# Kernel optimization log

Hardware: AMD Instinct MI355X
Metric: run time of the kernel (lower is better)

Reference implementation:

```python
import jax, jax.numpy as jnp
import numpy as np

NUM_HEADS = 8
CHANNELS = 512


def setup_inputs() -> dict:
    key = jax.random.key(0)
    k1, k2, k3, k4, k5 = jax.random.split(key, 5)
    C = CHANNELS
    x = jax.random.normal(k1, (8, C, 64, 64), dtype=jnp.float32)
    # 1x1 conv weights stored as (out_ch, in_ch) matrices
    qkv_w = jax.random.normal(k2, (3 * C, C), dtype=jnp.float32) * (C ** -0.5)
    qkv_b = jax.random.normal(k3, (3 * C,), dtype=jnp.float32) * 0.02
    proj_w = jax.random.normal(k4, (C, C), dtype=jnp.float32) * (C ** -0.5)
    proj_b = jax.random.normal(k5, (C,), dtype=jnp.float32) * 0.02
    return {"x": x, "qkv_w": qkv_w, "qkv_b": qkv_b, "proj_w": proj_w, "proj_b": proj_b}


def reference(x, qkv_w, qkv_b, proj_w, proj_b):
    B, C, H, W = x.shape
    heads = NUM_HEADS
    d = C // heads
    N = H * W
    scale = d ** -0.5
    # 1x1 conv == per-pixel matmul over channels
    qkv = jnp.einsum('bchw,oc->bohw', x, qkv_w) + qkv_b[None, :, None, None]
    qkv = qkv.reshape(B, 3, heads, d, N)
    q, k, v = qkv[:, 0], qkv[:, 1], qkv[:, 2]  # each (B, heads, d, N)
    # NOTE: attention over the channel dim -> (B, heads, d, d), as in the torch code
    attn = jax.nn.softmax(jnp.einsum('bhdn,bhen->bhde', q, k) * scale, axis=-1)
    # dropout is identity in eval mode
    out = jnp.einsum('bhde,bhen->bhdn', attn, v).reshape(B, C, H, W)
    out = jnp.einsum('bchw,oc->bohw', out, proj_w) + proj_b[None, :, None, None]
    return out, attn.mean(axis=1)  # (B,C,H,W), (B,d,d)
```

## Files before the change

### kernel.cpp

```cpp
#include <hip/hip_runtime.h>
#include <cstdio>
#include <cstdint>

#define BATCH 8
#define CH    512
#define OC3   1536
#define QKROWS 1024
#define NPIX  4096
#define HEADS 8
#define HDIM  64
#define KDEPTH 512
#define SCALE 0.125f
#define NSPLIT 16

typedef __bf16 bf16;
typedef __bf16 bf16x4 __attribute__((ext_vector_type(4)));
typedef __bf16 bf16x8 __attribute__((ext_vector_type(8)));
typedef float  f32x4  __attribute__((ext_vector_type(4)));

__global__ __launch_bounds__(256) void convert_bf16_kernel(
    const float* __restrict__ in, bf16* __restrict__ out, int n)
{
    const int i = blockIdx.x * 256 + threadIdx.x;
    if (i < n) out[i] = (bf16)in[i];
}

__global__ __launch_bounds__(256) void transpose_convert_kernel(
    const float* __restrict__ src, bf16* __restrict__ dst, size_t src_bstride)
{
    const int b  = blockIdx.z;
    const int n0 = blockIdx.x * 64;
    const int c0 = blockIdx.y * 64;
    __shared__ float tile[64][65];
    const int t = threadIdx.x;
    const float* xp = src + (size_t)b * src_bstride;

    #pragma unroll
    for (int i = 0; i < 4; ++i) {
        const int lin = t + 256 * i;
        const int r   = lin >> 4;
        const int c4  = (lin & 15) * 4;
        const float4 v = *(const float4*)(xp + (size_t)(c0 + r) * 4096 + n0 + c4);
        tile[r][c4 + 0] = v.x; tile[r][c4 + 1] = v.y;
        tile[r][c4 + 2] = v.z; tile[r][c4 + 3] = v.w;
    }
    __syncthreads();

    bf16* op = dst + (size_t)b * 4096 * 512;
    #pragma unroll
    for (int i = 0; i < 2; ++i) {
        const int lin = t + 256 * i;
        const int n   = lin >> 3;
        const int c8  = (lin & 7) * 8;
        bf16x8 v;
        #pragma unroll
        for (int jj = 0; jj < 8; ++jj) v[jj] = (bf16)tile[c8 + jj][n];
        *(bf16x8*)(op + (size_t)(n0 + n) * 512 + c0 + c8) = v;
    }
}

__global__ __launch_bounds__(256) void mfma_gemm_kernel(
    const bf16* __restrict__ A, const bf16* __restrict__ Bt,
    const float* __restrict__ bias, float* __restrict__ C,
    bf16* __restrict__ qkb, bf16* __restrict__ vt,
    int v_base, int c_rows, size_t a_bstride)
{
    const int b  = blockIdx.z;
    const int m0 = blockIdx.y * 128;
    const int n0 = blockIdx.x * 128;
    const bf16* Ap = A  + (size_t)b * a_bstride;
    const bf16* Bp = Bt + (size_t)b * NPIX * KDEPTH;

    __shared__ bf16 smem[16384];

    const int t    = threadIdx.x;
    const int lane = t & 63;
    const int wave = t >> 6;
    const int wr   = wave >> 1, wc = wave & 1;

    f32x4 acc[4][4];
    const f32x4 zf = {0.f, 0.f, 0.f, 0.f};
    #pragma unroll
    for (int i = 0; i < 4; ++i)
        #pragma unroll
        for (int j = 0; j < 4; ++j) acc[i][j] = zf;

    auto STAGE = [&](int p, int k0) {
        #pragma unroll
        for (int i = 0; i < 2; ++i) {
            const int c   = t + 256 * i;
            const int row = c >> 2;
            const int kb  = ((c & 3) ^ ((row >> 1) & 3)) * 8;
            __builtin_amdgcn_global_load_lds(
                (const __attribute__((address_space(1))) void*)(Ap + (size_t)(m0 + row) * KDEPTH + k0 + kb),
                (__attribute__((address_space(3))) void*)(smem + p * 8192 + c * 8), 16, 0, 0);
            __builtin_amdgcn_global_load_lds(
                (const __attribute__((address_space(1))) void*)(Bp + (size_t)(n0 + row) * KDEPTH + k0 + kb),
                (__attribute__((address_space(3))) void*)(smem + p * 8192 + 4096 + c * 8), 16, 0, 0);
        }
    };

    STAGE(0, 0);
    __syncthreads();
    int cur = 0;

    for (int kt = 0; kt < KDEPTH / 32; ++kt) {
        if (kt < KDEPTH / 32 - 1) STAGE(cur ^ 1, (kt + 1) * 32);

        const bf16* AsP = smem + cur * 8192;
        const bf16* BsP = AsP + 4096;
        bf16x8 af[4], bfv[4];
        #pragma unroll
        for (int i = 0; i < 4; ++i) {
            const int ar = wr * 64 + i * 16 + (lane & 15);
            const int ja = (lane >> 4) ^ ((ar >> 1) & 3);
            af[i]  = *(const bf16x8*)(AsP + ar * 32 + ja * 8);
            const int br = wc * 64 + i * 16 + (lane & 15);
            const int jb = (lane >> 4) ^ ((br >> 1) & 3);
            bfv[i] = *(const bf16x8*)(BsP + br * 32 + jb * 8);
        }
        #pragma unroll
        for (int i = 0; i < 4; ++i)
            #pragma unroll
            for (int j = 0; j < 4; ++j)
                acc[i][j] = __builtin_amdgcn_mfma_f32_16x16x32_bf16(
                    af[i], bfv[j], acc[i][j], 0, 0, 0);

        __syncthreads();
        cur ^= 1;
    }

    if (m0 >= v_base) {
        const int cbase = m0 - v_base;
        bf16* vb = vt + (size_t)b * NPIX * KDEPTH;
        bf16* tb = smem;
        #pragma unroll
        for (int p = 0; p < 2; ++p) {
            if (wc == p) {
                #pragma unroll
                for (int i = 0; i < 4; ++i) {
                    const int ml = wr * 64 + i * 16 + (lane >> 4) * 4;
                    #pragma unroll
                    for (int j = 0; j < 4; ++j) {
                        const int ns = j * 16 + (lane & 15);
                        bf16x4 pk;
                        #pragma unroll
                        for (int r = 0; r < 4; ++r)
                            pk[r] = (bf16)(acc[i][j][r] + bias[m0 + ml + r]);
                        *(bf16x4*)(tb + ns * 132 + ml) = pk;
                    }
                }
            }
            __syncthreads();
            #pragma unroll
            for (int ii = 0; ii < 4; ++ii) {
                const int lin = t + 256 * ii;
                const int row = lin >> 4;
                const int seg = lin & 15;
                const int4 v = *(const int4*)(tb + row * 132 + seg * 8);
                *(int4*)(vb + (size_t)(n0 + p * 64 + row) * KDEPTH + cbase + seg * 8) = v;
            }
            __syncthreads();
        }
    } else if (qkb) {
        bf16* Qp = qkb + (size_t)b * c_rows * NPIX;
        #pragma unroll
        for (int i = 0; i < 4; ++i) {
            const int mb = m0 + wr * 64 + i * 16 + (lane >> 4) * 4;
            #pragma unroll
            for (int r = 0; r < 4; ++r) {
                const int m  = mb + r;
                const float bv = bias[m];
                #pragma unroll
                for (int j = 0; j < 4; ++j) {
                    const int n = n0 + wc * 64 + j * 16 + (lane & 15);
                    Qp[(size_t)m * NPIX + n] = (bf16)(acc[i][j][r] + bv);
                }
            }
        }
    } else {
        float* Cp = C + (size_t)b * c_rows * NPIX;
        #pragma unroll
        for (int i = 0; i < 4; ++i) {
            const int mb = m0 + wr * 64 + i * 16 + (lane >> 4) * 4;
            #pragma unroll
            for (int r = 0; r < 4; ++r) {
                const int m  = mb + r;
                const float bv = bias[m];
                #pragma unroll
                for (int j = 0; j < 4; ++j) {
                    const int n = n0 + wc * 64 + j * 16 + (lane & 15);
                    Cp[(size_t)m * NPIX + n] = acc[i][j][r] + bv;
                }
            }
        }
    }
}

__global__ __launch_bounds__(256) void qk_partial_kernel(
    const bf16* __restrict__ qk, float* __restrict__ part)
{
    const int s  = blockIdx.x;
    const int bh = blockIdx.y;
    const int b = bh >> 3, h = bh & 7;
    const bf16* qbase = qk + ((size_t)b * QKROWS + h * HDIM) * NPIX;
    const bf16* kbase = qk + ((size_t)b * QKROWS + CH + h * HDIM) * NPIX;

    __shared__ bf16 smem[16384];

    const int t    = threadIdx.x;
    const int lane = t & 63;
    const int wave = t >> 6;

    f32x4 acc[4];
    const f32x4 zf = {0.f, 0.f, 0.f, 0.f};
    #pragma unroll
    for (int j = 0; j < 4; ++j) acc[j] = zf;

    auto STAGE = [&](int p, int n0) {
        #pragma unroll
        for (int i = 0; i < 2; ++i) {
            const int c   = t + 256 * i;
            const int row = c >> 3;
            const int nb  = ((c & 7) ^ (row & 7)) * 8;
            __builtin_amdgcn_global_load_lds(
                (const __attribute__((address_space(1))) void*)(qbase + (size_t)row * NPIX + n0 + nb),
                (__attribute__((address_space(3))) void*)(smem + p * 8192 + c * 8), 16, 0, 0);
            __builtin_amdgcn_global_load_lds(
                (const __attribute__((address_space(1))) void*)(kbase + (size_t)row * NPIX + n0 + nb),
                (__attribute__((address_space(3))) void*)(smem + p * 8192 + 4096 + c * 8), 16, 0, 0);
        }
    };

    STAGE(0, s * 256);
    __syncthreads();
    int cur = 0;

    for (int nc = 0; nc < 4; ++nc) {
        if (nc < 3) STAGE(cur ^ 1, s * 256 + (nc + 1) * 64);

        const bf16* Qs = smem + cur * 8192;
        const bf16* Ks = Qs + 4096;
        #pragma unroll
        for (int ks = 0; ks < 2; ++ks) {
            const int dr = wave * 16 + (lane & 15);
            const int ja = (ks * 4 + (lane >> 4)) ^ (dr & 7);
            const bf16x8 af = *(const bf16x8*)(Qs + dr * 64 + ja * 8);
            #pragma unroll
            for (int j = 0; j < 4; ++j) {
                const int er = j * 16 + (lane & 15);
                const int jb = (ks * 4 + (lane >> 4)) ^ (er & 7);
                const bf16x8 bf_ = *(const bf16x8*)(Ks + er * 64 + jb * 8);
                acc[j] = __builtin_amdgcn_mfma_f32_16x16x32_bf16(af, bf_, acc[j], 0, 0, 0);
            }
        }
        __syncthreads();
        cur ^= 1;
    }

    float* pb = part + (((size_t)bh * NSPLIT + s) * 64) * 64;
    #pragma unroll
    for (int j = 0; j < 4; ++j)
        #pragma unroll
        for (int r = 0; r < 4; ++r)
            pb[(size_t)(wave * 16 + (lane >> 4) * 4 + r) * 64 + j * 16 + (lane & 15)] = acc[j][r];
}

__global__ __launch_bounds__(256) void qk_reduce_softmax_kernel(
    const float* __restrict__ part, float* __restrict__ attn)
{
    const int bh = blockIdx.x;
    const int t  = threadIdx.x;
    const int r  = t >> 2;
    const int e0 = (t & 3) * 16;

    float v[16];
    #pragma unroll
    for (int i = 0; i < 16; ++i) v[i] = 0.f;

    const float* pb = part + ((size_t)bh * NSPLIT * 64) * 64 + r * 64 + e0;
    for (int s = 0; s < NSPLIT; ++s) {
        const float* ps = pb + (size_t)s * 4096;
        #pragma unroll
        for (int c4 = 0; c4 < 4; ++c4) {
            const float4 p = *(const float4*)(ps + c4 * 4);
            v[c4 * 4 + 0] += p.x; v[c4 * 4 + 1] += p.y;
            v[c4 * 4 + 2] += p.z; v[c4 * 4 + 3] += p.w;
        }
    }

    float m = -1e30f;
    #pragma unroll
    for (int i = 0; i < 16; ++i) m = fmaxf(m, v[i]);
    m = fmaxf(m, __shfl_xor(m, 1));
    m = fmaxf(m, __shfl_xor(m, 2));

    float sum = 0.f;
    #pragma unroll
    for (int i = 0; i < 16; ++i) {
        v[i] = __expf((v[i] - m) * SCALE);
        sum += v[i];
    }
    sum += __shfl_xor(sum, 1);
    sum += __shfl_xor(sum, 2);
    const float inv = 1.f / sum;

    float* arow = attn + ((size_t)bh * 64 + r) * 64 + e0;
    #pragma unroll
    for (int c4 = 0; c4 < 4; ++c4) {
        float4 o;
        o.x = v[c4 * 4 + 0] * inv; o.y = v[c4 * 4 + 1] * inv;
        o.z = v[c4 * 4 + 2] * inv; o.w = v[c4 * 4 + 3] * inv;
        *(float4*)(arow + c4 * 4) = o;
    }
}

__global__ __launch_bounds__(256) void attn_mean_kernel(
    const float* __restrict__ attn, float* __restrict__ om)
{
    const int idx = blockIdx.x * 256 + threadIdx.x;
    const int b = idx >> 12, de = idx & 4095;
    float s = 0.f;
    #pragma unroll
    for (int h = 0; h < 8; ++h)
        s += attn[(((size_t)b * 8 + h) << 12) + de];
    om[idx] = s * 0.125f;
}

__global__ __launch_bounds__(256) void wprime_kernel(
    const float* __restrict__ proj_w, const float* __restrict__ attn,
    bf16* __restrict__ wp)
{
    const int o0 = blockIdx.x * 64;
    const int h  = blockIdx.y;
    const int b  = blockIdx.z;

    __shared__ float ws[64][65];
    __shared__ float as_[64][65];

    const int t = threadIdx.x;
    #pragma unroll
    for (int i = 0; i < 4; ++i) {
        const int lin = t + 256 * i;
        const int r   = lin >> 4;
        const int c4  = (lin & 15) * 4;
        const float4 wv = *(const float4*)(proj_w + (size_t)(o0 + r) * CH + h * HDIM + c4);
        ws[r][c4 + 0] = wv.x; ws[r][c4 + 1] = wv.y;
        ws[r][c4 + 2] = wv.z; ws[r][c4 + 3] = wv.w;
        const float4 av = *(const float4*)(attn + (((size_t)(b * 8 + h) * 64) + r) * 64 + c4);
        as_[r][c4 + 0] = av.x; as_[r][c4 + 1] = av.y;
        as_[r][c4 + 2] = av.z; as_[r][c4 + 3] = av.w;
    }
    __syncthreads();

    const int tx = t & 15, ty = t >> 4;
    const int to = ty * 4, te = tx * 4;
    float acc[4][4] = {};
    for (int d = 0; d < 64; ++d) {
        float a[4], bb[4];
        #pragma unroll
        for (int i = 0; i < 4; ++i) a[i]  = ws[to + i][d];
        #pragma unroll
        for (int j = 0; j < 4; ++j) bb[j] = as_[d][te + j];
        #pragma unroll
        for (int i = 0; i < 4; ++i)
            #pragma unroll
            for (int j = 0; j < 4; ++j)
                acc[i][j] = fmaf(a[i], bb[j], acc[i][j]);
    }

    bf16* wb = wp + (size_t)b * CH * CH;
    #pragma unroll
    for (int i = 0; i < 4; ++i)
        #pragma unroll
        for (int j = 0; j < 4; ++j)
            wb[(size_t)(o0 + to + i) * CH + h * HDIM + te + j] = (bf16)acc[i][j];
}

extern "C" void kernel_launch(void* const* d_in, const int* in_sizes, int n_in,
                              void* d_out, int out_size, void* d_ws, size_t ws_size,
                              hipStream_t stream)
{
    (void)in_sizes; (void)n_in; (void)out_size;
    const float* x      = (const float*)d_in[0];
    const float* qkv_w  = (const float*)d_in[1];
    const float* qkv_b  = (const float*)d_in[2];
    const float* proj_w = (const float*)d_in[3];
    const float* proj_b = (const float*)d_in[4];

    float* out       = (float*)d_out;
    float* attn_mean = out + (size_t)BATCH * CH * NPIX;

    const size_t qk_bytes   = (size_t)BATCH * QKROWS * NPIX * 2;
    const size_t xt_bytes   = (size_t)BATCH * NPIX * KDEPTH * 2;
    const size_t vt_bytes   = (size_t)BATCH * NPIX * KDEPTH * 2;
    const size_t wq_bytes   = (size_t)OC3 * KDEPTH * 2;
    const size_t attn_bytes = (size_t)BATCH * HEADS * HDIM * HDIM * 4;
    const size_t part_bytes = (size_t)BATCH * HEADS * NSPLIT * HDIM * HDIM * 4;
    const size_t wp_bytes   = (size_t)BATCH * CH * CH * 2;
    const size_t need = qk_bytes + xt_bytes + vt_bytes + wq_bytes + attn_bytes + part_bytes + wp_bytes;
    if (ws_size < need) {
        fprintf(stderr, "[kernel_launch] ws_size=%zu < need=%zu — abort\n", ws_size, need);
        fflush(stderr);
        return;
    }

    char* p = (char*)d_ws;
    bf16*  qk     = (bf16*)p;             p += qk_bytes;
    bf16*  xt     = (bf16*)p;             p += xt_bytes;
    bf16*  vt     = (bf16*)p;             p += vt_bytes;
    bf16*  wq_b   = (bf16*)p;             p += wq_bytes;
    float* attn   = (float*)p;            p += attn_bytes;
    float* part   = (float*)p;            p += part_bytes;
    bf16*  wprime = (bf16*)p;

    convert_bf16_kernel<<<dim3((OC3 * KDEPTH + 255) / 256), 256, 0, stream>>>(
        qkv_w, wq_b, OC3 * KDEPTH);

    transpose_convert_kernel<<<dim3(NPIX / 64, KDEPTH / 64, BATCH), 256, 0, stream>>>(
        x, xt, (size_t)CH * NPIX);

    mfma_gemm_kernel<<<dim3(NPIX / 128, OC3 / 128, BATCH), 256, 0, stream>>>(
        wq_b, xt, qkv_b, nullptr, qk, vt, QKROWS, QKROWS, 0);

    qk_partial_kernel<<<dim3(NSPLIT, BATCH * HEADS), 256, 0, stream>>>(qk, part);
    qk_reduce_softmax_kernel<<<dim3(BATCH * HEADS), 256, 0, stream>>>(part, attn);

    attn_mean_kernel<<<dim3(BATCH * HDIM * HDIM / 256), 256, 0, stream>>>(attn, attn_mean);

    wprime_kernel<<<dim3(CH / 64, HEADS, BATCH), 256, 0, stream>>>(proj_w, attn, wprime);

    mfma_gemm_kernel<<<dim3(NPIX / 128, CH / 128, BATCH), 256, 0, stream>>>(
        wprime, vt, proj_b, out, nullptr, nullptr, 1 << 30, CH, (size_t)CH * CH);
}
```

Baseline: 161.5 us.

## Fold V projection into output weights to skip materializing V

Rather than computing V = Wv·x + bv and storing it transposed, the code builds per-batch W'' = W'·Wv with a small GEMM and a folded bias W'·bv + proj_b, then applies W'' directly to x in the final GEMM. This removes a third of the QKV GEMM and the write/read of the V tensor. In exchange it adds a per-batch 512x512x512 GEMM, a transpose of Wv, a bias kernel, and an extra bf16 rounding of the combined weights, which may cost some precision.

```diff
diff --git a/kernel.cpp b/kernel.cpp
--- a/kernel.cpp
+++ b/kernel.cpp
@@ -18,6 +18,9 @@
 typedef __bf16 bf16x8 __attribute__((ext_vector_type(8)));
 typedef float  f32x4  __attribute__((ext_vector_type(4)));
 
+#define AS1 __attribute__((address_space(1)))
+#define AS3 __attribute__((address_space(3)))
+
 __global__ __launch_bounds__(256) void convert_bf16_kernel(
     const float* __restrict__ in, bf16* __restrict__ out, int n)
 {
@@ -25,15 +28,43 @@
     if (i < n) out[i] = (bf16)in[i];
 }
 
+__global__ __launch_bounds__(256) void wvt_kernel(
+    const bf16* __restrict__ wv, bf16* __restrict__ wvt)
+{
+    const int c0 = blockIdx.x * 64;
+    const int d0 = blockIdx.y * 64;
+    __shared__ bf16 tl[64][72];
+    const int t = threadIdx.x;
+
+    #pragma unroll
+    for (int i = 0; i < 2; ++i) {
+        const int lin = t + 256 * i;
+        const int row = lin >> 3;
+        const int c8  = (lin & 7) * 8;
+        *(bf16x8*)&tl[row][c8] = *(const bf16x8*)(wv + (size_t)(d0 + row) * CH + c0 + c8);
+    }
+    __syncthreads();
+    #pragma unroll
+    for (int i = 0; i < 2; ++i) {
+        const int lin  = t + 256 * i;
+        const int crow = lin >> 3;
+        const int d8   = (lin & 7) * 8;
+        bf16x8 v;
+        #pragma unroll
+        for (int j = 0; j < 8; ++j) v[j] = tl[d8 + j][crow];
+        *(bf16x8*)(wvt + (size_t)(c0 + crow) * CH + d0 + d8) = v;
+    }
+}
+
 __global__ __launch_bounds__(256) void transpose_convert_kernel(
-    const float* __restrict__ src, bf16* __restrict__ dst, size_t src_bstride)
+    const float* __restrict__ src, bf16* __restrict__ dst)
 {
     const int b  = blockIdx.z;
     const int n0 = blockIdx.x * 64;
     const int c0 = blockIdx.y * 64;
     __shared__ float tile[64][65];
     const int t = threadIdx.x;
-    const float* xp = src + (size_t)b * src_bstride;
+    const float* xp = src + (size_t)b * CH * NPIX;
 
     #pragma unroll
     for (int i = 0; i < 4; ++i) {
@@ -46,7 +77,7 @@
     }
     __syncthreads();
 
-    bf16* op = dst + (size_t)b * 4096 * 512;
+    bf16* op = dst + (size_t)b * NPIX * CH;
     #pragma unroll
     for (int i = 0; i < 2; ++i) {
         const int lin = t + 256 * i;
@@ -55,20 +86,18 @@
         bf16x8 v;
         #pragma unroll
         for (int jj = 0; jj < 8; ++jj) v[jj] = (bf16)tile[c8 + jj][n];
-        *(bf16x8*)(op + (size_t)(n0 + n) * 512 + c0 + c8) = v;
-    }
-}
-
-__global__ __launch_bounds__(256) void mfma_gemm_kernel(
+        *(bf16x8*)(op + (size_t)(n0 + n) * CH + c0 + c8) = v;
+    }
+}
+
+__global__ __launch_bounds__(256) void gemm_qk_kernel(
     const bf16* __restrict__ A, const bf16* __restrict__ Bt,
-    const float* __restrict__ bias, float* __restrict__ C,
-    bf16* __restrict__ qkb, bf16* __restrict__ vt,
-    int v_base, int c_rows, size_t a_bstride)
+    const float* __restrict__ bias, bf16* __restrict__ qkb)
 {
     const int b  = blockIdx.z;
     const int m0 = blockIdx.y * 128;
     const int n0 = blockIdx.x * 128;
-    const bf16* Ap = A  + (size_t)b * a_bstride;
+    const bf16* Ap = A;
     const bf16* Bp = Bt + (size_t)b * NPIX * KDEPTH;
 
     __shared__ bf16 smem[16384];
@@ -92,11 +121,11 @@
             const int row = c >> 2;
             const int kb  = ((c & 3) ^ ((row >> 1) & 3)) * 8;
             __builtin_amdgcn_global_load_lds(
-                (const __attribute__((address_space(1))) void*)(Ap + (size_t)(m0 + row) * KDEPTH + k0 + kb),
-                (__attribute__((address_space(3))) void*)(smem + p * 8192 + c * 8), 16, 0, 0);
+                (const AS1 void*)(Ap + (size_t)(m0 + row) * KDEPTH + k0 + kb),
+                (AS3 void*)(smem + p * 8192 + c * 8), 16, 0, 0);
             __builtin_amdgcn_global_load_lds(
-                (const __attribute__((address_space(1))) void*)(Bp + (size_t)(n0 + row) * KDEPTH + k0 + kb),
-                (__attribute__((address_space(3))) void*)(smem + p * 8192 + 4096 + c * 8), 16, 0, 0);
+                (const AS1 void*)(Bp + (size_t)(n0 + row) * KDEPTH + k0 + kb),
+                (AS3 void*)(smem + p * 8192 + 4096 + c * 8), 16, 0, 0);
         }
     };
 
@@ -130,68 +159,18 @@
         cur ^= 1;
     }
 
-    if (m0 >= v_base) {
-        const int cbase = m0 - v_base;
-        bf16* vb = vt + (size_t)b * NPIX * KDEPTH;
-        bf16* tb = smem;
-        #pragma unroll
-        for (int p = 0; p < 2; ++p) {
-            if (wc == p) {
-                #pragma unroll
-                for (int i = 0; i < 4; ++i) {
-                    const int ml = wr * 64 + i * 16 + (lane >> 4) * 4;
-                    #pragma unroll
-                    for (int j = 0; j < 4; ++j) {
-                        const int ns = j * 16 + (lane & 15);
-                        bf16x4 pk;
-                        #pragma unroll
-                        for (int r = 0; r < 4; ++r)
-                            pk[r] = (bf16)(acc[i][j][r] + bias[m0 + ml + r]);
-                        *(bf16x4*)(tb + ns * 132 + ml) = pk;
-                    }
-                }
-            }
-            __syncthreads();
+    bf16* Qp = qkb + (size_t)b * QKROWS * NPIX;
+    #pragma unroll
+    for (int i = 0; i < 4; ++i) {
+        const int mb = m0 + wr * 64 + i * 16 + (lane >> 4) * 4;
+        #pragma unroll
+        for (int r = 0; r < 4; ++r) {
+            const int m  = mb + r;
+            const float bv = bias[m];
             #pragma unroll
-            for (int ii = 0; ii < 4; ++ii) {
-                const int lin = t + 256 * ii;
-                const int row = lin >> 4;
-                const int seg = lin & 15;
-                const int4 v = *(const int4*)(tb + row * 132 + seg * 8);
-                *(int4*)(vb + (size_t)(n0 + p * 64 + row) * KDEPTH + cbase + seg * 8) = v;
-            }
-            __syncthreads();
-        }
-    } else if (qkb) {
-        bf16* Qp = qkb + (size_t)b * c_rows * NPIX;
-        #pragma unroll
-        for (int i = 0; i < 4; ++i) {
-            const int mb = m0 + wr * 64 + i * 16 + (lane >> 4) * 4;
-            #pragma unroll
-            for (int r = 0; r < 4; ++r) {
-                const int m  = mb + r;
-                const float bv = bias[m];
-                #pragma unroll
-                for (int j = 0; j < 4; ++j) {
-                    const int n = n0 + wc * 64 + j * 16 + (lane & 15);
-                    Qp[(size_t)m * NPIX + n] = (bf16)(acc[i][j][r] + bv);
-                }
-            }
-        }
-    } else {
-        float* Cp = C + (size_t)b * c_rows * NPIX;
-        #pragma unroll
-        for (int i = 0; i < 4; ++i) {
-            const int mb = m0 + wr * 64 + i * 16 + (lane >> 4) * 4;
-            #pragma unroll
-            for (int r = 0; r < 4; ++r) {
-                const int m  = mb + r;
-                const float bv = bias[m];
-                #pragma unroll
-                for (int j = 0; j < 4; ++j) {
-                    const int n = n0 + wc * 64 + j * 16 + (lane & 15);
-                    Cp[(size_t)m * NPIX + n] = acc[i][j][r] + bv;
-                }
+            for (int j = 0; j < 4; ++j) {
+                const int n = n0 + wc * 64 + j * 16 + (lane & 15);
+                Qp[(size_t)m * NPIX + n] = (bf16)(acc[i][j][r] + bv);
             }
         }
     }
@@ -224,11 +203,11 @@
             const int row = c >> 3;
             const int nb  = ((c & 7) ^ (row & 7)) * 8;
             __builtin_amdgcn_global_load_lds(
-                (const __attribute__((address_space(1))) void*)(qbase + (size_t)row * NPIX + n0 + nb),
-                (__attribute__((address_space(3))) void*)(smem + p * 8192 + c * 8), 16, 0, 0);
+                (const AS1 void*)(qbase + (size_t)row * NPIX + n0 + nb),
+                (AS3 void*)(smem + p * 8192 + c * 8), 16, 0, 0);
             __builtin_amdgcn_global_load_lds(
-                (const __attribute__((address_space(1))) void*)(kbase + (size_t)row * NPIX + n0 + nb),
-                (__attribute__((address_space(3))) void*)(smem + p * 8192 + 4096 + c * 8), 16, 0, 0);
+                (const AS1 void*)(kbase + (size_t)row * NPIX + n0 + nb),
+                (AS3 void*)(smem + p * 8192 + 4096 + c * 8), 16, 0, 0);
         }
     };
 
@@ -377,6 +356,108 @@
             wb[(size_t)(o0 + to + i) * CH + h * HDIM + te + j] = (bf16)acc[i][j];
 }
 
+__global__ __launch_bounds__(256) void bias2_kernel(
+    const bf16* __restrict__ wp, const float* __restrict__ bv,
+    const float* __restrict__ pb, float* __restrict__ bias2)
+{
+    const int idx = blockIdx.x * 256 + threadIdx.x;
+    const int b = idx >> 9, o = idx & 511;
+    const bf16* wr = wp + ((size_t)b * CH + o) * CH;
+    float s = 0.f;
+    for (int d = 0; d < 512; ++d) s += (float)wr[d] * bv[d];
+    bias2[idx] = s + pb[o];
+}
+
+__global__ __launch_bounds__(256) void gemm128_kernel(
+    const bf16* __restrict__ A, const bf16* __restrict__ Bt,
+    const float* __restrict__ bias, size_t bias_bstride,
+    float* __restrict__ Cf, bf16* __restrict__ Cb,
+    int ncols, int c_rows, size_t a_bstride, size_t bt_bstride)
+{
+    const int b  = blockIdx.z;
+    const int m0 = blockIdx.y * 128;
+    const int n0 = blockIdx.x * 128;
+    const bf16* Ap = A  + (size_t)b * a_bstride;
+    const bf16* Bp = Bt + (size_t)b * bt_bstride;
+
+    __shared__ bf16 smem[16384];
+
+    const int t    = threadIdx.x;
+    const int lane = t & 63;
+    const int wave = t >> 6;
+    const int wr   = wave >> 1, wc = wave & 1;
+
+    f32x4 acc[4][4];
+    const f32x4 zf = {0.f, 0.f, 0.f, 0.f};
+    #pragma unroll
+    for (int i = 0; i < 4; ++i)
+        #pragma unroll
+        for (int j = 0; j < 4; ++j) acc[i][j] = zf;
+
+    auto STAGE = [&](int p, int k0) {
+        #pragma unroll
+        for (int i = 0; i < 2; ++i) {
+            const int c   = t + 256 * i;
+            const int row = c >> 2;
+            const int kb  = ((c & 3) ^ ((row >> 1) & 3)) * 8;
+            __builtin_amdgcn_global_load_lds(
+                (const AS1 void*)(Ap + (size_t)(m0 + row) * KDEPTH + k0 + kb),
+                (AS3 void*)(smem + p * 8192 + c * 8), 16, 0, 0);
+            __builtin_amdgcn_global_load_lds(
+                (const AS1 void*)(Bp + (size_t)(n0 + row) * KDEPTH + k0 + kb),
+                (AS3 void*)(smem + p * 8192 + 4096 + c * 8), 16, 0, 0);
+        }
+    };
+
+    STAGE(0, 0);
+    __syncthreads();
+    int cur = 0;
+
+    for (int kt = 0; kt < KDEPTH / 32; ++kt) {
+        if (kt < KDEPTH / 32 - 1) STAGE(cur ^ 1, (kt + 1) * 32);
+
+        const bf16* AsP = smem + cur * 8192;
+        const bf16* BsP = AsP + 4096;
+        bf16x8 af[4], bfv[4];
+        #pragma unroll
+        for (int i = 0; i < 4; ++i) {
+            const int ar = wr * 64 + i * 16 + (lane & 15);
+            const int ja = (lane >> 4) ^ ((ar >> 1) & 3);
+            af[i]  = *(const bf16x8*)(AsP + ar * 32 + ja * 8);
+            const int br = wc * 64 + i * 16 + (lane & 15);
+            const int jb = (lane >> 4) ^ ((br >> 1) & 3);
+            bfv[i] = *(const bf16x8*)(BsP + br * 32 + jb * 8);
+        }
+        #pragma unroll
+        for (int i = 0; i < 4; ++i)
+            #pragma unroll
+            for (int j = 0; j < 4; ++j)
+                acc[i][j] = __builtin_amdgcn_mfma_f32_16x16x32_bf16(
+                    af[i], bfv[j], acc[i][j], 0, 0, 0);
+
+        __syncthreads();
+        cur ^= 1;
+    }
+
+    #pragma unroll
+    for (int i = 0; i < 4; ++i) {
+        const int mb = m0 + wr * 64 + i * 16 + (lane >> 4) * 4;
+        #pragma unroll
+        for (int r = 0; r < 4; ++r) {
+            const int m  = mb + r;
+            const float bv = bias ? bias[b * bias_bstride + m] : 0.f;
+            #pragma unroll
+            for (int j = 0; j < 4; ++j) {
+                const int n = n0 + wc * 64 + j * 16 + (lane & 15);
+                if (Cb) Cb[(size_t)b * c_rows * ncols + (size_t)m * ncols + n] =
+                            (bf16)(acc[i][j][r] + bv);
+                else    Cf[(size_t)b * c_rows * ncols + (size_t)m * ncols + n] =
+                            acc[i][j][r] + bv;
+            }
+        }
+    }
+}
+
 extern "C" void kernel_launch(void* const* d_in, const int* in_sizes, int n_in,
                               void* d_out, int out_size, void* d_ws, size_t ws_size,
                               hipStream_t stream)
@@ -392,13 +473,16 @@
     float* attn_mean = out + (size_t)BATCH * CH * NPIX;
 
     const size_t qk_bytes   = (size_t)BATCH * QKROWS * NPIX * 2;
-    const size_t xt_bytes   = (size_t)BATCH * NPIX * KDEPTH * 2;
-    const size_t vt_bytes   = (size_t)BATCH * NPIX * KDEPTH * 2;
+    const size_t xt_bytes   = (size_t)BATCH * NPIX * CH * 2;
     const size_t wq_bytes   = (size_t)OC3 * KDEPTH * 2;
     const size_t attn_bytes = (size_t)BATCH * HEADS * HDIM * HDIM * 4;
     const size_t part_bytes = (size_t)BATCH * HEADS * NSPLIT * HDIM * HDIM * 4;
     const size_t wp_bytes   = (size_t)BATCH * CH * CH * 2;
-    const size_t need = qk_bytes + xt_bytes + vt_bytes + wq_bytes + attn_bytes + part_bytes + wp_bytes;
+    const size_t wpp_bytes  = (size_t)BATCH * CH * CH * 2;
+    const size_t wvt_bytes  = (size_t)CH * CH * 2;
+    const size_t b2_bytes   = (size_t)BATCH * CH * 4;
+    const size_t need = qk_bytes + xt_bytes + wq_bytes + attn_bytes + part_bytes +
+                        wp_bytes + wpp_bytes + wvt_bytes + b2_bytes;
     if (ws_size < need) {
         fprintf(stderr, "[kernel_launch] ws_size=%zu < need=%zu — abort\n", ws_size, need);
         fflush(stderr);
@@ -408,20 +492,22 @@
     char* p = (char*)d_ws;
     bf16*  qk     = (bf16*)p;             p += qk_bytes;
     bf16*  xt     = (bf16*)p;             p += xt_bytes;
-    bf16*  vt     = (bf16*)p;             p += vt_bytes;
     bf16*  wq_b   = (bf16*)p;             p += wq_bytes;
     float* attn   = (float*)p;            p += attn_bytes;
     float* part   = (float*)p;            p += part_bytes;
-    bf16*  wprime = (bf16*)p;
+    bf16*  wprime = (bf16*)p;             p += wp_bytes;
+    bf16*  wpp    = (bf16*)p;             p += wpp_bytes;
+    bf16*  wvt    = (bf16*)p;             p += wvt_bytes;
+    float* bias2  = (float*)p;
 
     convert_bf16_kernel<<<dim3((OC3 * KDEPTH + 255) / 256), 256, 0, stream>>>(
         qkv_w, wq_b, OC3 * KDEPTH);
-
-    transpose_convert_kernel<<<dim3(NPIX / 64, KDEPTH / 64, BATCH), 256, 0, stream>>>(
-        x, xt, (size_t)CH * NPIX);
-
-    mfma_gemm_kernel<<<dim3(NPIX / 128, OC3 / 128, BATCH), 256, 0, stream>>>(
-        wq_b, xt, qkv_b, nullptr, qk, vt, QKROWS, QKROWS, 0);
+    wvt_kernel<<<dim3(8, 8), 256, 0, stream>>>(wq_b + (size_t)2 * CH * KDEPTH, wvt);
+
+    transpose_convert_kernel<<<dim3(NPIX / 64, CH / 64, BATCH), 256, 0, stream>>>(x, xt);
+
+    gemm_qk_kernel<<<dim3(NPIX / 128, QKROWS / 128, BATCH), 256, 0, stream>>>(
+        wq_b, xt, qkv_b, qk);
 
     qk_partial_kernel<<<dim3(NSPLIT, BATCH * HEADS), 256, 0, stream>>>(qk, part);
     qk_reduce_softmax_kernel<<<dim3(BATCH * HEADS), 256, 0, stream>>>(part, attn);
@@ -430,6 +516,12 @@
 
     wprime_kernel<<<dim3(CH / 64, HEADS, BATCH), 256, 0, stream>>>(proj_w, attn, wprime);
 
-    mfma_gemm_kernel<<<dim3(NPIX / 128, CH / 128, BATCH), 256, 0, stream>>>(
-        wprime, vt, proj_b, out, nullptr, nullptr, 1 << 30, CH, (size_t)CH * CH);
-}
+    gemm128_kernel<<<dim3(CH / 128, CH / 128, BATCH), 256, 0, stream>>>(
+        wprime, wvt, nullptr, 0, nullptr, wpp, CH, CH, (size_t)CH * CH, 0);
+    bias2_kernel<<<dim3(BATCH * CH / 256), 256, 0, stream>>>(
+        wprime, qkv_b + 2 * CH, proj_b, bias2);
+
+    gemm128_kernel<<<dim3(NPIX / 128, CH / 128, BATCH), 256, 0, stream>>>(
+        wpp, xt, bias2, CH, out, nullptr, NPIX, CH, (size_t)CH * CH,
+        (size_t)NPIX * KDEPTH);
+}
```

After: 167.9 us. 4.0% more time.
